# Kernel tuning notes

Hardware: AMD Instinct MI355X
Metric: run time of the kernel (lower is better)

## Reference

```python
import jax, jax.numpy as jnp
import numpy as np

H = 1024      # hidden_size
V = 50257     # output_size (vocab)
L = 12        # max_length


def setup_inputs() -> dict:
    key = jax.random.key(0)
    ks = jax.random.split(key, 16)
    s = 0.02  # weight init scale
    return {
        "input_tok": jax.random.randint(ks[0], (1,), 0, V, dtype=jnp.int64) if jax.config.read('jax_enable_x64') else jax.random.randint(ks[0], (1,), 0, V, dtype=jnp.int32),
        "hidden": jax.random.normal(ks[1], (1, 1, H), jnp.float32),
        "encoder_outputs": jax.random.normal(ks[2], (L, H), jnp.float32),
        "emb": jax.random.normal(ks[3], (V, H), jnp.float32) * s,
        "attn_W": jax.random.normal(ks[4], (L, 2 * H), jnp.float32) * s,
        "attn_b": jnp.zeros((L,), jnp.float32),
        "comb_W": jax.random.normal(ks[5], (H, 2 * H), jnp.float32) * s,
        "comb_b": jnp.zeros((H,), jnp.float32),
        "Wih": jax.random.normal(ks[6], (H, H), jnp.float32) * s,
        "Whh": jax.random.normal(ks[7], (H, H), jnp.float32) * s,
        "bih": jnp.zeros((H,), jnp.float32),
        "bhh": jnp.zeros((H,), jnp.float32),
        "out_W": jax.random.normal(ks[8], (V, H), jnp.float32) * s,
        "out_b": jnp.zeros((V,), jnp.float32),
    }


def reference(input_tok, hidden, encoder_outputs, emb, attn_W, attn_b,
              comb_W, comb_b, Wih, Whh, bih, bhh, out_W, out_b):
    # embedding lookup -> [1, H]  (dropout = identity in eval mode)
    embedded = emb[input_tok[0]][None, :]
    h0 = hidden[0]  # [1, H]
    # Bahdanau-style attention over encoder_outputs [L, H]
    attn_in = jnp.concatenate([embedded, h0], axis=1)           # [1, 2H]
    attn_weights = jax.nn.softmax(attn_in @ attn_W.T + attn_b, axis=1)  # [1, L]
    attn_applied = attn_weights @ encoder_outputs               # [1, H]
    # combine + relu
    x = jnp.concatenate([embedded, attn_applied], axis=1)       # [1, 2H]
    x = jax.nn.relu(x @ comb_W.T + comb_b)                      # [1, H]
    # single vanilla-RNN (tanh) step
    h_new = jnp.tanh(x @ Wih.T + bih + h0 @ Whh.T + bhh)        # [1, H]
    # output projection + log_softmax over vocab
    logp = jax.nn.log_softmax(h_new @ out_W.T + out_b, axis=1)  # [1, V]
    return logp, h_new[None, :, :], attn_weights
```

## Files before the change

kernel.cpp:

```cpp
#include <hip/hip_runtime.h>
#include <hip/hip_bf16.h>
#include <math.h>

#define H 1024
#define V 50257
#define L 12

#define OFF_EMB    0
#define OFF_ATTN   1024
#define OFF_X      2048
#define OFF_H0     3072
#define OFF_H      4096
#define OFF_LOGITS 5120
#define OFF_SUM    (5120 + 50260)

__device__ __forceinline__ float wave_dot_f(const float* __restrict__ Wrow,
                                            const float* __restrict__ v, int K) {
    int lane = threadIdx.x & 63;
    float sum = 0.f;
    for (int c = 0; c < K; c += 256) {
        float4 w = ((const float4*)(Wrow + c))[lane];
        float4 a = ((const float4*)(v + c))[lane];
        sum += w.x * a.x + w.y * a.y + w.z * a.z + w.w * a.w;
    }
    for (int o = 32; o > 0; o >>= 1) sum += __shfl_down(sum, o);
    return sum;
}

__global__ void k1_attn(const int* tok_p, const float* hidden, const float* enc,
                        const float* emb, const float* attn_W, const float* attn_b,
                        float* ws, float* out) {
    __shared__ float att_in[2 * H];
    __shared__ float red[256];
    __shared__ float wsm[L];
    int t = threadIdx.x;
    int tok = tok_p[0];
    const float* erow = emb + (size_t)tok * H;
    for (int j = t; j < H; j += 256) {
        float e  = erow[j];
        float h0 = hidden[j];
        att_in[j]       = e;
        att_in[H + j]   = h0;
        ws[OFF_EMB + j] = e;
        ws[OFF_H0 + j]  = h0;
    }
    if (t == 0) ws[OFF_SUM] = 0.f;
    __syncthreads();
    for (int l = 0; l < L; ++l) {
        float p = 0.f;
        const float* wr = attn_W + l * 2 * H;
        for (int j = t; j < 2 * H; j += 256) p += att_in[j] * wr[j];
        red[t] = p;
        __syncthreads();
        for (int s = 128; s > 0; s >>= 1) {
            if (t < s) red[t] += red[t + s];
            __syncthreads();
        }
        if (t == 0) wsm[l] = red[0] + attn_b[l];
        __syncthreads();
    }
    if (t == 0) {
        float m = wsm[0];
        for (int l = 1; l < L; ++l) m = fmaxf(m, wsm[l]);
        float s = 0.f;
        for (int l = 0; l < L; ++l) { wsm[l] = expf(wsm[l] - m); s += wsm[l]; }
        float inv = 1.f / s;
        for (int l = 0; l < L; ++l) {
            wsm[l] *= inv;
            out[V + H + l] = wsm[l];
        }
    }
    __syncthreads();
    for (int hh = t; hh < H; hh += 256) {
        float a = 0.f;
        for (int l = 0; l < L; ++l) a += wsm[l] * enc[l * H + hh];
        ws[OFF_ATTN + hh] = a;
    }
}

__global__ void k2_combine(const float* comb_W, const float* comb_b, float* ws) {
    int wave = threadIdx.x >> 6;
    int row = blockIdx.x * 4 + wave;
    float d = wave_dot_f(comb_W + (size_t)row * 2 * H, ws + OFF_EMB, 2 * H);
    if ((threadIdx.x & 63) == 0) {
        ws[OFF_X + row] = fmaxf(d + comb_b[row], 0.f);
    }
}

__global__ void k3_rnn(const float* Wih, const float* Whh, const float* bih,
                       const float* bhh, float* ws, float* out) {
    int wave = threadIdx.x >> 6;
    int row = blockIdx.x * 4 + wave;
    float d = wave_dot_f(Wih + (size_t)row * H, ws + OFF_X, H)
            + wave_dot_f(Whh + (size_t)row * H, ws + OFF_H0, H);
    if ((threadIdx.x & 63) == 0) {
        float h = tanhf(d + bih[row] + bhh[row]);
        ws[OFF_H + row] = h;
        out[V + row] = h;
    }
}

#define K4_BLOCKS 1024
__global__ void k4_outproj(const float* out_W, const float* out_b, float* ws) {
    __shared__ float sexp[4];
    int wave = threadIdx.x >> 6;
    int lane = threadIdx.x & 63;
    float esum = 0.f;
    for (int row = blockIdx.x * 4 + wave; row < V; row += K4_BLOCKS * 4) {
        float d = wave_dot_f(out_W + (size_t)row * H, ws + OFF_H, H) + out_b[row];
        if (lane == 0) {
            ws[OFF_LOGITS + row] = d;
            esum += expf(d);
        }
    }
    if (lane == 0) sexp[wave] = esum;
    __syncthreads();
    if (threadIdx.x == 0)
        atomicAdd(ws + OFF_SUM, sexp[0] + sexp[1] + sexp[2] + sexp[3]);
}

__global__ void k5_norm(const float* ws, float* out) {
    int v = blockIdx.x * 256 + threadIdx.x;
    if (v < V) {
        float lse = logf(ws[OFF_SUM]);
        out[v] = ws[OFF_LOGITS + v] - lse;
    }
}

extern "C" void kernel_launch(void* const* d_in, const int* in_sizes, int n_in,
                              void* d_out, int out_size, void* d_ws, size_t ws_size,
                              hipStream_t stream) {
    const int*   tok    = (const int*)d_in[0];
    const float* hidden = (const float*)d_in[1];
    const float* enc    = (const float*)d_in[2];
    const float* emb    = (const float*)d_in[3];
    const float* attn_W = (const float*)d_in[4];
    const float* attn_b = (const float*)d_in[5];
    const float* comb_W = (const float*)d_in[6];
    const float* comb_b = (const float*)d_in[7];
    const float* Wih    = (const float*)d_in[8];
    const float* Whh    = (const float*)d_in[9];
    const float* bih    = (const float*)d_in[10];
    const float* bhh    = (const float*)d_in[11];
    const float* out_W  = (const float*)d_in[12];
    const float* out_b  = (const float*)d_in[13];
    float* ws  = (float*)d_ws;
    float* out = (float*)d_out;

    k1_attn   <<<1,                256, 0, stream>>>(tok, hidden, enc, emb, attn_W, attn_b, ws, out);
    k2_combine<<<H / 4,            256, 0, stream>>>(comb_W, comb_b, ws);
    k3_rnn    <<<H / 4,            256, 0, stream>>>(Wih, Whh, bih, bhh, ws, out);
    k4_outproj<<<K4_BLOCKS,        256, 0, stream>>>(out_W, out_b, ws);
    k5_norm   <<<(V + 255) / 256,  256, 0, stream>>>(ws, out);
}
```

Baseline: 433.7 us.

## Fuse all decoder stages into one cooperative kernel with grid syncs

Replaces the five separate kernel launches with a single cooperative kernel of 1024 blocks that separates the attention, combine, RNN, output projection and normalization phases with grid-wide syncs. The combine and RNN stages now assign one row per block with a block-level reduction, and the attention reduction uses wave shuffles instead of a shared-memory tree. This aims to remove launch gaps and inter-kernel drain between dependent stages. In exchange it adds four grid barriers, and it depends on all 1024 blocks being co-resident.

```diff
diff --git a/kernel.cpp b/kernel.cpp
--- a/kernel.cpp
+++ b/kernel.cpp
@@ -1,10 +1,13 @@
 #include <hip/hip_runtime.h>
-#include <hip/hip_bf16.h>
+#include <hip/hip_cooperative_groups.h>
 #include <math.h>
 
 #define H 1024
 #define V 50257
 #define L 12
+#define GRID 1024
+
+namespace cg = cooperative_groups;
 
 #define OFF_EMB    0
 #define OFF_ATTN   1024
@@ -14,116 +17,149 @@
 #define OFF_LOGITS 5120
 #define OFF_SUM    (5120 + 50260)
 
-__device__ __forceinline__ float wave_dot_f(const float* __restrict__ Wrow,
-                                            const float* __restrict__ v, int K) {
-    int lane = threadIdx.x & 63;
-    float sum = 0.f;
-    for (int c = 0; c < K; c += 256) {
-        float4 w = ((const float4*)(Wrow + c))[lane];
-        float4 a = ((const float4*)(v + c))[lane];
-        sum += w.x * a.x + w.y * a.y + w.z * a.z + w.w * a.w;
-    }
-    for (int o = 32; o > 0; o >>= 1) sum += __shfl_down(sum, o);
-    return sum;
+__device__ __forceinline__ float dot4(float4 a, float4 b) {
+    return a.x * b.x + a.y * b.y + a.z * b.z + a.w * b.w;
 }
 
-__global__ void k1_attn(const int* tok_p, const float* hidden, const float* enc,
-                        const float* emb, const float* attn_W, const float* attn_b,
-                        float* ws, float* out) {
+__device__ __forceinline__ float wave_red(float s) {
+    for (int o = 32; o > 0; o >>= 1) s += __shfl_down(s, o);
+    return s;
+}
+
+__global__ __launch_bounds__(256, 4) void fused_decoder(
+    const int* __restrict__ tok_p, const float* __restrict__ hidden,
+    const float* __restrict__ enc, const float* __restrict__ emb,
+    const float* __restrict__ attn_W, const float* __restrict__ attn_b,
+    const float* __restrict__ comb_W, const float* __restrict__ comb_b,
+    const float* __restrict__ Wih, const float* __restrict__ Whh,
+    const float* __restrict__ bih, const float* __restrict__ bhh,
+    const float* __restrict__ out_W, const float* __restrict__ out_b,
+    float* __restrict__ ws, float* __restrict__ out)
+{
+    cg::grid_group grid = cg::this_grid();
     __shared__ float att_in[2 * H];
-    __shared__ float red[256];
+    __shared__ float red[4];
     __shared__ float wsm[L];
-    int t = threadIdx.x;
-    int tok = tok_p[0];
-    const float* erow = emb + (size_t)tok * H;
-    for (int j = t; j < H; j += 256) {
-        float e  = erow[j];
-        float h0 = hidden[j];
-        att_in[j]       = e;
-        att_in[H + j]   = h0;
-        ws[OFF_EMB + j] = e;
-        ws[OFF_H0 + j]  = h0;
-    }
-    if (t == 0) ws[OFF_SUM] = 0.f;
-    __syncthreads();
-    for (int l = 0; l < L; ++l) {
-        float p = 0.f;
-        const float* wr = attn_W + l * 2 * H;
-        for (int j = t; j < 2 * H; j += 256) p += att_in[j] * wr[j];
-        red[t] = p;
+    __shared__ float bc;
+    const int t = threadIdx.x;
+    const int wave = t >> 6;
+    const int lane = t & 63;
+
+    if (blockIdx.x == 0) {
+        const int tok = tok_p[0];
+        const float* erow = emb + (size_t)tok * H;
+        for (int j = t; j < H; j += 256) {
+            float e  = erow[j];
+            float h0 = hidden[j];
+            att_in[j]       = e;
+            att_in[H + j]   = h0;
+            ws[OFF_EMB + j] = e;
+            ws[OFF_H0 + j]  = h0;
+        }
+        if (t == 0) ws[OFF_SUM] = 0.f;
         __syncthreads();
-        for (int s = 128; s > 0; s >>= 1) {
-            if (t < s) red[t] += red[t + s];
+        for (int l = 0; l < L; ++l) {
+            float p = 0.f;
+            const float* wr = attn_W + l * 2 * H;
+            for (int j = t; j < 2 * H; j += 256) p += att_in[j] * wr[j];
+            p = wave_red(p);
+            if (lane == 0) red[wave] = p;
+            __syncthreads();
+            if (t == 0) wsm[l] = red[0] + red[1] + red[2] + red[3] + attn_b[l];
             __syncthreads();
         }
-        if (t == 0) wsm[l] = red[0] + attn_b[l];
+        if (t == 0) {
+            float m = wsm[0];
+            for (int l = 1; l < L; ++l) m = fmaxf(m, wsm[l]);
+            float s = 0.f;
+            for (int l = 0; l < L; ++l) { wsm[l] = expf(wsm[l] - m); s += wsm[l]; }
+            float inv = 1.f / s;
+            for (int l = 0; l < L; ++l) {
+                wsm[l] *= inv;
+                out[V + H + l] = wsm[l];
+            }
+        }
+        __syncthreads();
+        for (int hh = t; hh < H; hh += 256) {
+            float a = 0.f;
+            for (int l = 0; l < L; ++l) a += wsm[l] * enc[l * H + hh];
+            ws[OFF_ATTN + hh] = a;
+        }
+    }
+    __threadfence();
+    grid.sync();
+    __threadfence();
+
+    {
+        const int row = blockIdx.x;
+        const float4* Wr = (const float4*)(comb_W + (size_t)row * 2 * H);
+        const float4* vv = (const float4*)(ws + OFF_EMB);
+        float s = dot4(Wr[t], vv[t]) + dot4(Wr[t + 256], vv[t + 256]);
+        s = wave_red(s);
+        if (lane == 0) red[wave] = s;
+        __syncthreads();
+        if (t == 0)
+            ws[OFF_X + row] = fmaxf(red[0] + red[1] + red[2] + red[3] + comb_b[row], 0.f);
+    }
+    __threadfence();
+    grid.sync();
+    __threadfence();
+
+    {
+        const int row = blockIdx.x;
+        const float4* Wi = (const float4*)(Wih + (size_t)row * H);
+        const float4* Wh = (const float4*)(Whh + (size_t)row * H);
+        const float4* xv = (const float4*)(ws + OFF_X);
+        const float4* hv = (const float4*)(ws + OFF_H0);
+        float s = dot4(Wi[t], xv[t]) + dot4(Wh[t], hv[t]);
+        s = wave_red(s);
+        if (lane == 0) red[wave] = s;
+        __syncthreads();
+        if (t == 0) {
+            float h = tanhf(red[0] + red[1] + red[2] + red[3] + bih[row] + bhh[row]);
+            ws[OFF_H + row] = h;
+            out[V + row] = h;
+        }
         __syncthreads();
     }
-    if (t == 0) {
-        float m = wsm[0];
-        for (int l = 1; l < L; ++l) m = fmaxf(m, wsm[l]);
-        float s = 0.f;
-        for (int l = 0; l < L; ++l) { wsm[l] = expf(wsm[l] - m); s += wsm[l]; }
-        float inv = 1.f / s;
-        for (int l = 0; l < L; ++l) {
-            wsm[l] *= inv;
-            out[V + H + l] = wsm[l];
+    __threadfence();
+    grid.sync();
+    __threadfence();
+
+    {
+        float esum = 0.f;
+        const float* hvec = ws + OFF_H;
+        for (int row = blockIdx.x * 4 + wave; row < V; row += GRID * 4) {
+            const float4* Wr = (const float4*)(out_W + (size_t)row * H);
+            const float4* hv = (const float4*)hvec;
+            float s = dot4(Wr[lane], hv[lane]) + dot4(Wr[lane + 64], hv[lane + 64])
+                    + dot4(Wr[lane + 128], hv[lane + 128]) + dot4(Wr[lane + 192], hv[lane + 192]);
+            s = wave_red(s);
+            if (lane == 0) {
+                float d = s + out_b[row];
+                ws[OFF_LOGITS + row] = d;
+                esum += expf(d);
+            }
         }
+        if (lane == 0) red[wave] = esum;
+        __syncthreads();
+        if (t == 0)
+            atomicAdd(ws + OFF_SUM, red[0] + red[1] + red[2] + red[3]);
     }
-    __syncthreads();
-    for (int hh = t; hh < H; hh += 256) {
-        float a = 0.f;
-        for (int l = 0; l < L; ++l) a += wsm[l] * enc[l * H + hh];
-        ws[OFF_ATTN + hh] = a;
-    }
-}
+    __threadfence();
+    grid.sync();
+    __threadfence();
 
-__global__ void k2_combine(const float* comb_W, const float* comb_b, float* ws) {
-    int wave = threadIdx.x >> 6;
-    int row = blockIdx.x * 4 + wave;
-    float d = wave_dot_f(comb_W + (size_t)row * 2 * H, ws + OFF_EMB, 2 * H);
-    if ((threadIdx.x & 63) == 0) {
-        ws[OFF_X + row] = fmaxf(d + comb_b[row], 0.f);
-    }
-}
-
-__global__ void k3_rnn(const float* Wih, const float* Whh, const float* bih,
-                       const float* bhh, float* ws, float* out) {
-    int wave = threadIdx.x >> 6;
-    int row = blockIdx.x * 4 + wave;
-    float d = wave_dot_f(Wih + (size_t)row * H, ws + OFF_X, H)
-            + wave_dot_f(Whh + (size_t)row * H, ws + OFF_H0, H);
-    if ((threadIdx.x & 63) == 0) {
-        float h = tanhf(d + bih[row] + bhh[row]);
-        ws[OFF_H + row] = h;
-        out[V + row] = h;
-    }
-}
-
-#define K4_BLOCKS 1024
-__global__ void k4_outproj(const float* out_W, const float* out_b, float* ws) {
-    __shared__ float sexp[4];
-    int wave = threadIdx.x >> 6;
-    int lane = threadIdx.x & 63;
-    float esum = 0.f;
-    for (int row = blockIdx.x * 4 + wave; row < V; row += K4_BLOCKS * 4) {
-        float d = wave_dot_f(out_W + (size_t)row * H, ws + OFF_H, H) + out_b[row];
-        if (lane == 0) {
-            ws[OFF_LOGITS + row] = d;
-            esum += expf(d);
+    {
+        if (t == 0) {
+            float se = __hip_atomic_load(ws + OFF_SUM, __ATOMIC_RELAXED,
+                                         __HIP_MEMORY_SCOPE_AGENT);
+            bc = logf(se);
         }
-    }
-    if (lane == 0) sexp[wave] = esum;
-    __syncthreads();
-    if (threadIdx.x == 0)
-        atomicAdd(ws + OFF_SUM, sexp[0] + sexp[1] + sexp[2] + sexp[3]);
-}
-
-__global__ void k5_norm(const float* ws, float* out) {
-    int v = blockIdx.x * 256 + threadIdx.x;
-    if (v < V) {
-        float lse = logf(ws[OFF_SUM]);
-        out[v] = ws[OFF_LOGITS + v] - lse;
+        __syncthreads();
+        const float lse = bc;
+        const int idx = blockIdx.x * 256 + t;
+        if (idx < V) out[idx] = ws[OFF_LOGITS + idx] - lse;
     }
 }
 
@@ -147,9 +183,10 @@
     float* ws  = (float*)d_ws;
     float* out = (float*)d_out;
 
-    k1_attn   <<<1,                256, 0, stream>>>(tok, hidden, enc, emb, attn_W, attn_b, ws, out);
-    k2_combine<<<H / 4,            256, 0, stream>>>(comb_W, comb_b, ws);
-    k3_rnn    <<<H / 4,            256, 0, stream>>>(Wih, Whh, bih, bhh, ws, out);
-    k4_outproj<<<K4_BLOCKS,        256, 0, stream>>>(out_W, out_b, ws);
-    k5_norm   <<<(V + 255) / 256,  256, 0, stream>>>(ws, out);
+    void* args[] = { (void*)&tok, (void*)&hidden, (void*)&enc, (void*)&emb,
+                     (void*)&attn_W, (void*)&attn_b, (void*)&comb_W, (void*)&comb_b,
+                     (void*)&Wih, (void*)&Whh, (void*)&bih, (void*)&bhh,
+                     (void*)&out_W, (void*)&out_b, (void*)&ws, (void*)&out };
+    hipLaunchCooperativeKernel((void*)fused_decoder, dim3(GRID), dim3(256),
+                               args, 0, stream);
 }
```

Measured after the change: 1.462 ms. +237.2%, slower.
